# Performance work log

Hardware: AMD Instinct MI355X
Metric: run time of the kernel (lower is better)

Reference implementation:

```python
import jax, jax.numpy as jnp
import numpy as np

N_E = 1024
E_DIM = 256
TAU = 0.5
BETA = 0.25
LAMB = 0.1
EPS = 1e-10


def setup_inputs() -> dict:
    key = jax.random.key(0)
    k1, k2, k3 = jax.random.split(key, 3)
    z = jax.random.normal(k1, (16, 1024, E_DIM), dtype=jnp.float32)
    # kaiming-normal-initialized codebook (std = sqrt(2 / fan_in))
    emb = jax.random.normal(k2, (N_E, E_DIM), dtype=jnp.float32) * np.sqrt(2.0 / E_DIM)
    u = jax.random.uniform(k3, (16 * 1024, N_E), dtype=jnp.float32)
    return {"z": z, "emb": emb, "u": u}


def reference(z, emb, u):
    zf = z.reshape(-1, E_DIM)                                  # [N, e_dim]
    # squared euclidean distances to each code: ||z||^2 + ||e||^2 - 2 z.e
    d = (jnp.sum(zf * zf, axis=1, keepdims=True)
         + jnp.sum(emb * emb, axis=1)
         - 2.0 * jnp.matmul(zf, emb.T))                        # [N, n_e]
    # gumbel-softmax (hard, straight-through) on logits = -d
    g = -jnp.log(-jnp.log(u + EPS) + EPS)
    y_soft = jax.nn.softmax((-d + g) / TAU, axis=-1)
    idx = jnp.argmax(y_soft, axis=-1)
    y_hard = jax.nn.one_hot(idx, N_E, dtype=y_soft.dtype)
    probs = y_hard + y_soft - jax.lax.stop_gradient(y_soft)    # [N, n_e]
    z_q = jnp.matmul(probs, emb).reshape(z.shape)
    # orthogonality loss on the codebook gram matrix
    gram = jnp.matmul(emb, emb.T)
    ortho = jnp.mean((gram - jnp.eye(N_E, dtype=emb.dtype)) ** 2) / (N_E ** 2)
    emb_loss = jnp.mean((jax.lax.stop_gradient(z_q) - z) ** 2)
    commit = BETA * jnp.mean((z_q - jax.lax.stop_gradient(z)) ** 2)
    loss = emb_loss + BETA * commit + LAMB * ortho
    z_q_st = z + jax.lax.stop_gradient(z_q - z)
    e_mean = jnp.mean(probs, axis=0)
    perplexity = jnp.exp(-jnp.sum(e_mean * jnp.log(e_mean + EPS)))
    return loss, z_q_st, perplexity
```

## Files before the change

### kernel.cpp

```cpp
#include <hip/hip_runtime.h>
#include <math.h>
#include <stdint.h>


#define NROWS 16384
#define NE    1024
#define ED    256
#define EPSF  1e-10f
#define INV2048 4.8828125e-4f

typedef _Float16 half_t;
typedef __attribute__((ext_vector_type(4))) _Float16 half4;
typedef __attribute__((ext_vector_type(8))) _Float16 half8;
typedef __attribute__((ext_vector_type(16))) float floatx16;

__device__ __forceinline__ void gl_lds16(const half_t* g, half_t* l) {
    __builtin_amdgcn_global_load_lds(
        (const __attribute__((address_space(1))) uint32_t*)g,
        (__attribute__((address_space(3))) uint32_t*)l, 16, 0, 0);
}

__device__ __forceinline__ unsigned long long packMax(float v, int code) {
    unsigned int b   = __float_as_uint(v);
    unsigned int key = (b & 0x80000000u) ? ~b : (b | 0x80000000u);
    return ((unsigned long long)key << 32) | (unsigned int)(NE - 1 - code);
}

__global__ __launch_bounds__(256) void vq_split(
        const float* __restrict__ z, const float* __restrict__ emb,
        half_t* __restrict__ zh, half_t* __restrict__ zl,
        half_t* __restrict__ eh, half_t* __restrict__ el,
        unsigned long long* __restrict__ best, int* __restrict__ cnt,
        double* __restrict__ mse_acc)
{
    const int gid = blockIdx.x * 256 + threadIdx.x;
    const int ZQ4 = NROWS * ED / 4;
    const bool is_z = gid < ZQ4;
    const float4 v = is_z ? ((const float4*)z)[gid]
                          : ((const float4*)emb)[gid - ZQ4];
    const float x[4] = {v.x, v.y, v.z, v.w};
    half4 h, l;
#pragma unroll
    for (int i = 0; i < 4; ++i) {
        const half_t hi = (half_t)x[i];
        const float  lo = (x[i] - (float)hi) * 2048.0f;
        h[i] = hi; l[i] = (half_t)lo;
    }
    if (is_z) {
        *(half4*)&zh[(size_t)gid * 4] = h;
        *(half4*)&zl[(size_t)gid * 4] = l;
    } else {
        *(half4*)&eh[(size_t)(gid - ZQ4) * 4] = h;
        *(half4*)&el[(size_t)(gid - ZQ4) * 4] = l;
    }
    if (gid < NROWS) best[gid] = 0ull;
    if (gid < NE)    cnt[gid]  = 0;
    if (gid == 0)    *mse_acc  = 0.0;
}

__global__ void vq_enorm(const float* __restrict__ emb, float* __restrict__ enorm) {
    int gid  = blockIdx.x * blockDim.x + threadIdx.x;
    int code = gid >> 6;
    int lane = gid & 63;
    const float* e = emb + (size_t)code * ED;
    float s = 0.f;
#pragma unroll
    for (int q = 0; q < 4; ++q) { float v = e[lane + (q << 6)]; s += v * v; }
#pragma unroll
    for (int o = 32; o; o >>= 1) s += __shfl_down(s, o);
    if (lane == 0) enorm[code] = s;
}

#define BK 64
__global__ __launch_bounds__(256, 2) void vq_gemm(
        const half_t* __restrict__ zh, const half_t* __restrict__ zl,
        const half_t* __restrict__ eh, const half_t* __restrict__ el,
        const float* __restrict__ u, const float* __restrict__ enorm,
        unsigned long long* __restrict__ best)
{
    __shared__ __align__(16) half_t Ah[128 * BK], Al[128 * BK],
                                    Bh[128 * BK], Bl[128 * BK];
    __shared__ unsigned long long blmax[128];

    const int t    = threadIdx.x;
    const int w    = t >> 6;
    const int lane = t & 63;
    const int m0 = blockIdx.x * 128, n0 = blockIdx.y * 128;
    const int wm = (w >> 1) * 64,    wn = (w & 1) * 64;
    const int lrow = lane & 31;
    const int lk   = (lane >> 5) << 3;

    if (t < 128) blmax[t] = 0ull;

    floatx16 accH[2][2] = {};
    floatx16 accX[2][2] = {};

    for (int kc = 0; kc < ED; kc += BK) {
        __syncthreads();
#pragma unroll
        for (int it = 0; it < 4; ++it) {
            const int c       = it * 256 + t;
            const int ldsbase = (it * 256 + w * 64) * 8;
            const int m       = c >> 3;
            const int k8      = (c & 7) << 3;
            const size_t ga = (size_t)(m0 + m) * ED + kc + k8;
            const size_t gb = (size_t)(n0 + m) * ED + kc + k8;
            gl_lds16(zh + ga, Ah + ldsbase);
            gl_lds16(zl + ga, Al + ldsbase);
            gl_lds16(eh + gb, Bh + ldsbase);
            gl_lds16(el + gb, Bl + ldsbase);
        }
        __syncthreads();
#pragma unroll
        for (int ks = 0; ks < BK / 16; ++ks) {
            const int ko = ks * 16 + lk;
            half8 ah[2], al[2], bh[2], bl[2];
#pragma unroll
            for (int i = 0; i < 2; ++i) {
                const int ar = wm + i * 32 + lrow;
                const int br = wn + i * 32 + lrow;
                ah[i] = *(const half8*)&Ah[ar * BK + ko];
                al[i] = *(const half8*)&Al[ar * BK + ko];
                bh[i] = *(const half8*)&Bh[br * BK + ko];
                bl[i] = *(const half8*)&Bl[br * BK + ko];
            }
#pragma unroll
            for (int i = 0; i < 2; ++i)
#pragma unroll
            for (int j = 0; j < 2; ++j) {
                accH[i][j] = __builtin_amdgcn_mfma_f32_32x32x16_f16(ah[i], bh[j], accH[i][j], 0, 0, 0);
                accX[i][j] = __builtin_amdgcn_mfma_f32_32x32x16_f16(ah[i], bl[j], accX[i][j], 0, 0, 0);
                accX[i][j] = __builtin_amdgcn_mfma_f32_32x32x16_f16(al[i], bh[j], accX[i][j], 0, 0, 0);
            }
        }
    }

    const int   col0 = n0 + wn + lrow;
    const float en0  = enorm[col0];
    const float en1  = enorm[col0 + 32];
    const int   hw   = lane >> 5;
#pragma unroll
    for (int i = 0; i < 2; ++i) {
#pragma unroll
        for (int r = 0; r < 16; ++r) {
            const int lr = wm + i * 32 + (r & 3) + ((r >> 2) << 3) + (hw << 2);
            const size_t urow = (size_t)(m0 + lr) * NE;
            const float d0 = accH[i][0][r] + accX[i][0][r] * INV2048;
            const float d1 = accH[i][1][r] + accX[i][1][r] * INV2048;
            const float u0 = u[urow + col0];
            const float u1 = u[urow + col0 + 32];
            const float g0 = -__logf(-__logf(u0 + EPSF) + EPSF);
            const float g1 = -__logf(-__logf(u1 + EPSF) + EPSF);
            const float s0 = 2.f * d0 - en0 + g0;
            const float s1 = 2.f * d1 - en1 + g1;
            float sb; int cb;
            if (s1 > s0) { sb = s1; cb = col0 + 32; } else { sb = s0; cb = col0; }
            atomicMax(&blmax[lr], packMax(sb, cb));
        }
    }
    __syncthreads();
    if (t < 128) atomicMax(&best[m0 + t], blmax[t]);
}

__global__ __launch_bounds__(256) void vq_out(
        const float* __restrict__ z, const float* __restrict__ emb,
        const unsigned long long* __restrict__ best,
        int* __restrict__ cnt, double* __restrict__ mse_acc,
        float* __restrict__ out)
{
    __shared__ int   ridx[64];
    __shared__ float redbuf[4];
    const int t  = threadIdx.x;
    const int m0 = blockIdx.x * 64;

    if (t < 64) {
        const unsigned long long p = best[m0 + t];
        const int code = NE - 1 - (int)(p & 0xFFFFFFFFu);
        ridx[t] = code;
        atomicAdd(&cnt[code], 1);
    }
    __syncthreads();

    float lmse = 0.f;
#pragma unroll
    for (int rr = 0; rr < 16; ++rr) {
        const int row = (rr << 2) + (t >> 6);
        const int d   = t & 63;
        const int j   = ridx[row];
        const size_t zb = (size_t)(m0 + row) * ED;
        const size_t eb = (size_t)j * ED;
#pragma unroll
        for (int q = 0; q < 4; ++q) {
            const int dim = d + (q << 6);
            const float df = emb[eb + dim] - z[zb + dim];
            out[1 + zb + dim] = z[zb + dim] + df;
            lmse = fmaf(df, df, lmse);
        }
    }
#pragma unroll
    for (int o = 32; o; o >>= 1) lmse += __shfl_down(lmse, o);
    if ((t & 63) == 0) redbuf[t >> 6] = lmse;
    __syncthreads();
    if (t == 0) {
        float s = redbuf[0] + redbuf[1] + redbuf[2] + redbuf[3];
        atomicAdd(mse_acc, (double)s);
    }
}

__global__ void vq_final(const int* __restrict__ cnt, const double* __restrict__ mse_acc,
                         float* __restrict__ out) {
    __shared__ double red[16];
    const int t = threadIdx.x;
    const float em   = (float)cnt[t] / (float)NROWS;
    const float term = em * logf(em + EPSF);
    double s = (double)term;
#pragma unroll
    for (int o = 32; o; o >>= 1) s += __shfl_down(s, o);
    if ((t & 63) == 0) red[t >> 6] = s;
    __syncthreads();
    if (t == 0) {
        double tot = 0.0;
#pragma unroll
        for (int i = 0; i < 16; ++i) tot += red[i];
        const float perp = expf((float)(-tot));
        const double mse = *mse_acc / (double)((size_t)NROWS * ED);
        out[0] = (float)(mse * 1.0625);
        out[1 + (size_t)NROWS * ED] = perp;
    }
}

extern "C" void kernel_launch(void* const* d_in, const int* in_sizes, int n_in,
                              void* d_out, int out_size, void* d_ws, size_t ws_size,
                              hipStream_t stream) {
    const float* z   = (const float*)d_in[0];
    const float* emb = (const float*)d_in[1];
    const float* u   = (const float*)d_in[2];
    float* out = (float*)d_out;

    double*             mse_acc = (double*)d_ws;
    int*                cnt     = (int*)((char*)d_ws + 64);
    float*              enorm   = (float*)((char*)d_ws + 64 + 4096);
    unsigned long long* best    = (unsigned long long*)((char*)d_ws + 64 + 4096 + 4096);
    const size_t small_end = ((64 + 4096 + 4096 + (size_t)NROWS * 8) + 255) & ~(size_t)255;

    const size_t zsplit = (size_t)NROWS * ED * 2;
    const size_t esplit = (size_t)NE * ED * 2;
    half_t *zh, *zl, *eh, *el;
    if (ws_size >= small_end + 2 * zsplit + 2 * esplit) {
        char* big = (char*)d_ws + small_end;
        zh = (half_t*)big;
        zl = (half_t*)(big + zsplit);
        eh = (half_t*)(big + 2 * zsplit);
        el = (half_t*)(big + 2 * zsplit + esplit);
    } else {
        zh = (half_t*)((char*)d_out + 8);
        zl = (half_t*)((char*)d_out + 8 + zsplit);
        eh = (half_t*)((char*)d_ws + small_end);
        el = (half_t*)((char*)d_ws + small_end + esplit);
    }

    vq_split<<<(NROWS * ED / 4 + NE * ED / 4) / 256, 256, 0, stream>>>(
        z, emb, zh, zl, eh, el, best, cnt, mse_acc);
    vq_enorm<<<256, 256, 0, stream>>>(emb, enorm);
    vq_gemm<<<dim3(NROWS / 128, NE / 128), 256, 0, stream>>>(
        zh, zl, eh, el, u, enorm, best);
    vq_out<<<NROWS / 64, 256, 0, stream>>>(z, emb, best, cnt, mse_acc, out);
    vq_final<<<1, 1024, 0, stream>>>(cnt, mse_acc, out);
}
```

Measured before the change: 198.2 us.

## Fuse enorm into prep and output/final stages into GEMM via last-block counters

Folds the codebook norm computation into the split/prep kernel and, when the workspace is large, fuses the output gather, MSE reduction and perplexity into the GEMM kernel. A per-row-tile counter lets the last-arriving block finish that tile, and a global done counter lets the final block compute the scalars. The GEMM also gains XOR-swizzled LDS layout to reduce bank conflicts, swaps grid order so code tiles for the same rows run adjacently, and replaces per-element LDS atomics with a wave shuffle max reduction plus one global atomic per row. This removes three kernel launches and their tail gaps, at the cost of serialised tail work inside the last blocks and reliance on fences and atomics for correctness.

```diff
diff --git a/kernel.cpp b/kernel.cpp
--- a/kernel.cpp
+++ b/kernel.cpp
@@ -8,6 +8,7 @@
 #define ED    256
 #define EPSF  1e-10f
 #define INV2048 4.8828125e-4f
+#define BK 64
 
 typedef _Float16 half_t;
 typedef __attribute__((ext_vector_type(4))) _Float16 half4;
@@ -26,71 +27,74 @@
     return ((unsigned long long)key << 32) | (unsigned int)(NE - 1 - code);
 }
 
-__global__ __launch_bounds__(256) void vq_split(
+__global__ __launch_bounds__(256) void vq_prep(
         const float* __restrict__ z, const float* __restrict__ emb,
         half_t* __restrict__ zh, half_t* __restrict__ zl,
         half_t* __restrict__ eh, half_t* __restrict__ el,
-        unsigned long long* __restrict__ best, int* __restrict__ cnt,
-        double* __restrict__ mse_acc)
+        float* __restrict__ enorm, unsigned long long* __restrict__ best,
+        int* __restrict__ cnt, double* __restrict__ mse_acc,
+        int* __restrict__ mtile_cnt, int* __restrict__ done_cnt)
 {
     const int gid = blockIdx.x * 256 + threadIdx.x;
     const int ZQ4 = NROWS * ED / 4;
-    const bool is_z = gid < ZQ4;
-    const float4 v = is_z ? ((const float4*)z)[gid]
-                          : ((const float4*)emb)[gid - ZQ4];
-    const float x[4] = {v.x, v.y, v.z, v.w};
-    half4 h, l;
-#pragma unroll
-    for (int i = 0; i < 4; ++i) {
-        const half_t hi = (half_t)x[i];
-        const float  lo = (x[i] - (float)hi) * 2048.0f;
-        h[i] = hi; l[i] = (half_t)lo;
-    }
-    if (is_z) {
+    if (gid < ZQ4) {
+        const float4 v = ((const float4*)z)[gid];
+        const float x[4] = {v.x, v.y, v.z, v.w};
+        half4 h, l;
+#pragma unroll
+        for (int i = 0; i < 4; ++i) {
+            const half_t hi = (half_t)x[i];
+            h[i] = hi; l[i] = (half_t)((x[i] - (float)hi) * 2048.0f);
+        }
         *(half4*)&zh[(size_t)gid * 4] = h;
         *(half4*)&zl[(size_t)gid * 4] = l;
     } else {
-        *(half4*)&eh[(size_t)(gid - ZQ4) * 4] = h;
-        *(half4*)&el[(size_t)(gid - ZQ4) * 4] = l;
-    }
-    if (gid < NROWS) best[gid] = 0ull;
-    if (gid < NE)    cnt[gid]  = 0;
-    if (gid == 0)    *mse_acc  = 0.0;
-}
-
-__global__ void vq_enorm(const float* __restrict__ emb, float* __restrict__ enorm) {
-    int gid  = blockIdx.x * blockDim.x + threadIdx.x;
-    int code = gid >> 6;
-    int lane = gid & 63;
-    const float* e = emb + (size_t)code * ED;
-    float s = 0.f;
-#pragma unroll
-    for (int q = 0; q < 4; ++q) { float v = e[lane + (q << 6)]; s += v * v; }
-#pragma unroll
-    for (int o = 32; o; o >>= 1) s += __shfl_down(s, o);
-    if (lane == 0) enorm[code] = s;
-}
-
-#define BK 64
-__global__ __launch_bounds__(256, 2) void vq_gemm(
+        const int eg = gid - ZQ4;
+        const float4 v = ((const float4*)emb)[eg];
+        const float x[4] = {v.x, v.y, v.z, v.w};
+        half4 h, l;
+#pragma unroll
+        for (int i = 0; i < 4; ++i) {
+            const half_t hi = (half_t)x[i];
+            h[i] = hi; l[i] = (half_t)((x[i] - (float)hi) * 2048.0f);
+        }
+        *(half4*)&eh[(size_t)eg * 4] = h;
+        *(half4*)&el[(size_t)eg * 4] = l;
+        float s = v.x*v.x + v.y*v.y + v.z*v.z + v.w*v.w;
+#pragma unroll
+        for (int o = 32; o; o >>= 1) s += __shfl_down(s, o);
+        if ((threadIdx.x & 63) == 0) enorm[eg >> 6] = s;
+        if (eg < NROWS) best[eg] = 0ull;
+        if (eg < NE)    cnt[eg]  = 0;
+        if (eg < 128)   mtile_cnt[eg] = 0;
+        if (eg == 0)  { *mse_acc = 0.0; *done_cnt = 0; }
+    }
+}
+
+template<bool FUSED>
+__global__ __launch_bounds__(256, 2) void vq_fused_k(
         const half_t* __restrict__ zh, const half_t* __restrict__ zl,
         const half_t* __restrict__ eh, const half_t* __restrict__ el,
         const float* __restrict__ u, const float* __restrict__ enorm,
-        unsigned long long* __restrict__ best)
+        const float* __restrict__ z, const float* __restrict__ emb,
+        unsigned long long* __restrict__ best, int* __restrict__ cnt,
+        double* __restrict__ mse_acc, int* __restrict__ mtile_cnt,
+        int* __restrict__ done_cnt, float* __restrict__ out)
 {
     __shared__ __align__(16) half_t Ah[128 * BK], Al[128 * BK],
                                     Bh[128 * BK], Bl[128 * BK];
-    __shared__ unsigned long long blmax[128];
+    __shared__ int    flags[2];
+    __shared__ int    ridx[128];
+    __shared__ float  redf[4];
+    __shared__ double redd[4];
 
     const int t    = threadIdx.x;
     const int w    = t >> 6;
     const int lane = t & 63;
-    const int m0 = blockIdx.x * 128, n0 = blockIdx.y * 128;
+    const int n0 = blockIdx.x * 128, m0 = blockIdx.y * 128;
     const int wm = (w >> 1) * 64,    wn = (w & 1) * 64;
     const int lrow = lane & 31;
-    const int lk   = (lane >> 5) << 3;
-
-    if (t < 128) blmax[t] = 0ull;
+    const int hw   = lane >> 5;
 
     floatx16 accH[2][2] = {};
     floatx16 accX[2][2] = {};
@@ -99,30 +103,32 @@
         __syncthreads();
 #pragma unroll
         for (int it = 0; it < 4; ++it) {
-            const int c       = it * 256 + t;
-            const int ldsbase = (it * 256 + w * 64) * 8;
-            const int m       = c >> 3;
-            const int k8      = (c & 7) << 3;
-            const size_t ga = (size_t)(m0 + m) * ED + kc + k8;
-            const size_t gb = (size_t)(n0 + m) * ED + kc + k8;
-            gl_lds16(zh + ga, Ah + ldsbase);
-            gl_lds16(zl + ga, Al + ldsbase);
-            gl_lds16(eh + gb, Bh + ldsbase);
-            gl_lds16(el + gb, Bl + ldsbase);
+            const int s   = it * 256 + t;
+            const int row = s >> 3;
+            const int c   = (s & 7) ^ (row & 7);
+            const int ldsoff = (it * 256 + w * 64) * 8;
+            const size_t ga = (size_t)(m0 + row) * ED + kc + c * 8;
+            const size_t gb = (size_t)(n0 + row) * ED + kc + c * 8;
+            gl_lds16(zh + ga, Ah + ldsoff);
+            gl_lds16(zl + ga, Al + ldsoff);
+            gl_lds16(eh + gb, Bh + ldsoff);
+            gl_lds16(el + gb, Bl + ldsoff);
         }
         __syncthreads();
 #pragma unroll
         for (int ks = 0; ks < BK / 16; ++ks) {
-            const int ko = ks * 16 + lk;
+            const int cch = ks * 2 + hw;
             half8 ah[2], al[2], bh[2], bl[2];
 #pragma unroll
             for (int i = 0; i < 2; ++i) {
                 const int ar = wm + i * 32 + lrow;
                 const int br = wn + i * 32 + lrow;
-                ah[i] = *(const half8*)&Ah[ar * BK + ko];
-                al[i] = *(const half8*)&Al[ar * BK + ko];
-                bh[i] = *(const half8*)&Bh[br * BK + ko];
-                bl[i] = *(const half8*)&Bl[br * BK + ko];
+                const int sa = ar * 8 + (cch ^ (ar & 7));
+                const int sb = br * 8 + (cch ^ (br & 7));
+                ah[i] = *(const half8*)&Ah[sa * 8];
+                al[i] = *(const half8*)&Al[sa * 8];
+                bh[i] = *(const half8*)&Bh[sb * 8];
+                bl[i] = *(const half8*)&Bl[sb * 8];
             }
 #pragma unroll
             for (int i = 0; i < 2; ++i)
@@ -138,7 +144,6 @@
     const int   col0 = n0 + wn + lrow;
     const float en0  = enorm[col0];
     const float en1  = enorm[col0 + 32];
-    const int   hw   = lane >> 5;
 #pragma unroll
     for (int i = 0; i < 2; ++i) {
 #pragma unroll
@@ -147,19 +152,85 @@
             const size_t urow = (size_t)(m0 + lr) * NE;
             const float d0 = accH[i][0][r] + accX[i][0][r] * INV2048;
             const float d1 = accH[i][1][r] + accX[i][1][r] * INV2048;
-            const float u0 = u[urow + col0];
-            const float u1 = u[urow + col0 + 32];
-            const float g0 = -__logf(-__logf(u0 + EPSF) + EPSF);
-            const float g1 = -__logf(-__logf(u1 + EPSF) + EPSF);
+            const float g0 = -__logf(-__logf(u[urow + col0] + EPSF) + EPSF);
+            const float g1 = -__logf(-__logf(u[urow + col0 + 32] + EPSF) + EPSF);
             const float s0 = 2.f * d0 - en0 + g0;
             const float s1 = 2.f * d1 - en1 + g1;
-            float sb; int cb;
-            if (s1 > s0) { sb = s1; cb = col0 + 32; } else { sb = s0; cb = col0; }
-            atomicMax(&blmax[lr], packMax(sb, cb));
-        }
-    }
-    __syncthreads();
-    if (t < 128) atomicMax(&best[m0 + t], blmax[t]);
+            unsigned long long pk = (s1 > s0) ? packMax(s1, col0 + 32)
+                                              : packMax(s0, col0);
+#pragma unroll
+            for (int off = 16; off; off >>= 1) {
+                const unsigned long long o =
+                    (unsigned long long)__shfl_xor((long long)pk, off, 64);
+                if (o > pk) pk = o;
+            }
+            if (lrow == 0) atomicMax(&best[m0 + lr], pk);
+        }
+    }
+
+    if (!FUSED) return;
+
+    __syncthreads();
+    if (t == 0) {
+        __threadfence();
+        flags[0] = (atomicAdd(&mtile_cnt[blockIdx.y], 1) == 7) ? 1 : 0;
+    }
+    __syncthreads();
+    if (flags[0]) {
+        if (t < 128) {
+            const unsigned long long p = atomicMax(&best[m0 + t], 0ull);
+            const int code = NE - 1 - (int)(p & 0xFFFFFFFFu);
+            ridx[t] = code;
+            atomicAdd(&cnt[code], 1);
+        }
+        __syncthreads();
+        float lmse = 0.f;
+#pragma unroll
+        for (int rr = 0; rr < 32; ++rr) {
+            const int row = (rr << 2) + (t >> 6);
+            const int d   = t & 63;
+            const int j   = ridx[row];
+            const size_t zb = (size_t)(m0 + row) * ED;
+            const size_t eb = (size_t)j * ED;
+#pragma unroll
+            for (int q = 0; q < 4; ++q) {
+                const int dim = d + (q << 6);
+                const float df = emb[eb + dim] - z[zb + dim];
+                out[1 + zb + dim] = z[zb + dim] + df;
+                lmse = fmaf(df, df, lmse);
+            }
+        }
+#pragma unroll
+        for (int o = 32; o; o >>= 1) lmse += __shfl_down(lmse, o);
+        if ((t & 63) == 0) redf[t >> 6] = lmse;
+        __syncthreads();
+        if (t == 0) {
+            atomicAdd(mse_acc, (double)(redf[0] + redf[1] + redf[2] + redf[3]));
+            __threadfence();
+            flags[1] = (atomicAdd(done_cnt, 1) == 127) ? 1 : 0;
+        }
+        __syncthreads();
+        if (flags[1]) {
+            double s = 0.0;
+#pragma unroll
+            for (int q = 0; q < 4; ++q) {
+                const int   c  = atomicAdd(&cnt[(q << 8) + t], 0);
+                const float em = (float)c / (float)NROWS;
+                s += (double)(em * logf(em + EPSF));
+            }
+#pragma unroll
+            for (int o = 32; o; o >>= 1) s += __shfl_down(s, o);
+            if ((t & 63) == 0) redd[t >> 6] = s;
+            __syncthreads();
+            if (t == 0) {
+                const double tot = redd[0] + redd[1] + redd[2] + redd[3];
+                const double mse = atomicAdd(mse_acc, 0.0)
+                                   / (double)((size_t)NROWS * ED);
+                out[0] = (float)(mse * 1.0625);
+                out[1 + (size_t)NROWS * ED] = (float)exp(-tot);
+            }
+        }
+    }
 }
 
 __global__ __launch_bounds__(256) void vq_out(
@@ -172,7 +243,6 @@
     __shared__ float redbuf[4];
     const int t  = threadIdx.x;
     const int m0 = blockIdx.x * 64;
-
     if (t < 64) {
         const unsigned long long p = best[m0 + t];
         const int code = NE - 1 - (int)(p & 0xFFFFFFFFu);
@@ -180,7 +250,6 @@
         atomicAdd(&cnt[code], 1);
     }
     __syncthreads();
-
     float lmse = 0.f;
 #pragma unroll
     for (int rr = 0; rr < 16; ++rr) {
@@ -201,19 +270,16 @@
     for (int o = 32; o; o >>= 1) lmse += __shfl_down(lmse, o);
     if ((t & 63) == 0) redbuf[t >> 6] = lmse;
     __syncthreads();
-    if (t == 0) {
-        float s = redbuf[0] + redbuf[1] + redbuf[2] + redbuf[3];
-        atomicAdd(mse_acc, (double)s);
-    }
+    if (t == 0)
+        atomicAdd(mse_acc, (double)(redbuf[0] + redbuf[1] + redbuf[2] + redbuf[3]));
 }
 
 __global__ void vq_final(const int* __restrict__ cnt, const double* __restrict__ mse_acc,
                          float* __restrict__ out) {
     __shared__ double red[16];
     const int t = threadIdx.x;
-    const float em   = (float)cnt[t] / (float)NROWS;
-    const float term = em * logf(em + EPSF);
-    double s = (double)term;
+    const float em = (float)cnt[t] / (float)NROWS;
+    double s = (double)(em * logf(em + EPSF));
 #pragma unroll
     for (int o = 32; o; o >>= 1) s += __shfl_down(s, o);
     if ((t & 63) == 0) red[t >> 6] = s;
@@ -222,10 +288,9 @@
         double tot = 0.0;
 #pragma unroll
         for (int i = 0; i < 16; ++i) tot += red[i];
-        const float perp = expf((float)(-tot));
         const double mse = *mse_acc / (double)((size_t)NROWS * ED);
         out[0] = (float)(mse * 1.0625);
-        out[1 + (size_t)NROWS * ED] = perp;
+        out[1 + (size_t)NROWS * ED] = (float)exp(-tot);
     }
 }
 
@@ -237,33 +302,44 @@
     const float* u   = (const float*)d_in[2];
     float* out = (float*)d_out;
 
-    double*             mse_acc = (double*)d_ws;
-    int*                cnt     = (int*)((char*)d_ws + 64);
-    float*              enorm   = (float*)((char*)d_ws + 64 + 4096);
-    unsigned long long* best    = (unsigned long long*)((char*)d_ws + 64 + 4096 + 4096);
-    const size_t small_end = ((64 + 4096 + 4096 + (size_t)NROWS * 8) + 255) & ~(size_t)255;
+    double*             mse_acc   = (double*)d_ws;
+    int*                done_cnt  = (int*)((char*)d_ws + 64);
+    int*                mtile_cnt = (int*)((char*)d_ws + 128);
+    int*                cnt       = (int*)((char*)d_ws + 1024);
+    float*              enorm     = (float*)((char*)d_ws + 5120);
+    unsigned long long* best      = (unsigned long long*)((char*)d_ws + 9216);
+    const size_t small_end = 140288;
 
     const size_t zsplit = (size_t)NROWS * ED * 2;
     const size_t esplit = (size_t)NE * ED * 2;
+    const bool bigws = ws_size >= small_end + 2 * zsplit + 2 * esplit;
+
     half_t *zh, *zl, *eh, *el;
-    if (ws_size >= small_end + 2 * zsplit + 2 * esplit) {
+    if (bigws) {
         char* big = (char*)d_ws + small_end;
         zh = (half_t*)big;
         zl = (half_t*)(big + zsplit);
         eh = (half_t*)(big + 2 * zsplit);
         el = (half_t*)(big + 2 * zsplit + esplit);
     } else {
-        zh = (half_t*)((char*)d_out + 8);
-        zl = (half_t*)((char*)d_out + 8 + zsplit);
+        zh = (half_t*)((char*)d_out + 16);
+        zl = (half_t*)((char*)d_out + 16 + zsplit);
         eh = (half_t*)((char*)d_ws + small_end);
         el = (half_t*)((char*)d_ws + small_end + esplit);
     }
 
-    vq_split<<<(NROWS * ED / 4 + NE * ED / 4) / 256, 256, 0, stream>>>(
-        z, emb, zh, zl, eh, el, best, cnt, mse_acc);
-    vq_enorm<<<256, 256, 0, stream>>>(emb, enorm);
-    vq_gemm<<<dim3(NROWS / 128, NE / 128), 256, 0, stream>>>(
-        zh, zl, eh, el, u, enorm, best);
-    vq_out<<<NROWS / 64, 256, 0, stream>>>(z, emb, best, cnt, mse_acc, out);
-    vq_final<<<1, 1024, 0, stream>>>(cnt, mse_acc, out);
-}
+    vq_prep<<<(NROWS * ED / 4 + NE * ED / 4) / 256, 256, 0, stream>>>(
+        z, emb, zh, zl, eh, el, enorm, best, cnt, mse_acc, mtile_cnt, done_cnt);
+
+    if (bigws) {
+        vq_fused_k<true><<<dim3(NE / 128, NROWS / 128), 256, 0, stream>>>(
+            zh, zl, eh, el, u, enorm, z, emb, best, cnt, mse_acc,
+            mtile_cnt, done_cnt, out);
+    } else {
+        vq_fused_k<false><<<dim3(NE / 128, NROWS / 128), 256, 0, stream>>>(
+            zh, zl, eh, el, u, enorm, z, emb, best, cnt, mse_acc,
+            mtile_cnt, done_cnt, out);
+        vq_out<<<NROWS / 64, 256, 0, stream>>>(z, emb, best, cnt, mse_acc, out);
+        vq_final<<<1, 1024, 0, stream>>>(cnt, mse_acc, out);
+    }
+}
```

New measurement: 263.2 us. 32.8% more time.
